# Kernel tuning notes

Measured on AMD Instinct MI355X. Metric: run time of the kernel, lower is better.

## Reference

```python
import jax, jax.numpy as jnp
import numpy as np

L = 4          # num_layers
D = 512        # d_model
NH = 8         # num_heads
DH = 64        # d_head
DFF = 2048     # d_ff
EPS = 1e-5     # nn.LayerNorm default eps


def _layer_norm(x, g, b):
    m = x.mean(axis=-1, keepdims=True)
    v = ((x - m) ** 2).mean(axis=-1, keepdims=True)
    return (x - m) / jnp.sqrt(v + EPS) * g + b


def setup_inputs() -> dict:
    key = jax.random.key(0)
    ks = jax.random.split(key, 14)
    s = 0.02
    z = jax.random.normal(ks[0], (4, 16, D, 8, 8), dtype=jnp.float32)
    Wq = s * jax.random.normal(ks[1], (L, D, NH * DH), dtype=jnp.float32)
    Wk = s * jax.random.normal(ks[2], (L, D, NH * DH), dtype=jnp.float32)
    Wv = s * jax.random.normal(ks[3], (L, D, NH * DH), dtype=jnp.float32)
    Wo = s * jax.random.normal(ks[4], (L, NH * DH, D), dtype=jnp.float32)
    W1 = s * jax.random.normal(ks[5], (L, D, DFF), dtype=jnp.float32)
    b1 = jnp.zeros((L, DFF), dtype=jnp.float32)
    W2 = s * jax.random.normal(ks[6], (L, DFF, D), dtype=jnp.float32)
    b2 = jnp.zeros((L, D), dtype=jnp.float32)
    ln1_g = jnp.ones((L, D), dtype=jnp.float32)
    ln1_b = jnp.zeros((L, D), dtype=jnp.float32)
    ln2_g = jnp.ones((L, D), dtype=jnp.float32)
    ln2_b = jnp.zeros((L, D), dtype=jnp.float32)
    return {"z": z, "Wq": Wq, "Wk": Wk, "Wv": Wv, "Wo": Wo,
            "W1": W1, "b1": b1, "W2": W2, "b2": b2,
            "ln1_g": ln1_g, "ln1_b": ln1_b, "ln2_g": ln2_g, "ln2_b": ln2_b}


def _forward(z, Wq, Wk, Wv, Wo, W1, b1, W2, b2, ln1_g, ln1_b, ln2_g, ln2_b):
    B, T, Dm, H, W = z.shape
    N = H * W
    Tp = T * N  # T' = t*h*w
    # sinusoidal positional embedding over T' positions
    pos = jnp.arange(Tp, dtype=z.dtype)
    inv_freq = 1.0 / (10000.0 ** (jnp.arange(0, Dm, 2, dtype=z.dtype) / Dm))
    si = pos[:, None] * inv_freq[None, :]                 # (T', D/2)
    pos_emb = jnp.concatenate([jnp.sin(si), jnp.cos(si)], axis=-1)[:, None, :]  # (T',1,D)
    # rearrange 'b t d h w -> (t h w) b d'
    x = jnp.transpose(z, (1, 3, 4, 0, 2)).reshape(Tp, B, Dm)
    x = x + pos_emb
    # block-causal mask at block size N (True = masked)
    blk = jnp.arange(Tp) // N
    mask = blk[None, :] > blk[:, None]                    # (T'_q, T'_k)
    scale = 1.0 / np.sqrt(DH)
    outs = []
    for l in range(L):
        # post-lnorm multi-head attention (LN applied before residual add)
        q = (x @ Wq[l]).reshape(Tp, B, NH, DH)
        k = (x @ Wk[l]).reshape(Tp, B, NH, DH)
        v = (x @ Wv[l]).reshape(Tp, B, NH, DH)
        s = jnp.einsum('ibnd,jbnd->ijbn', q, k) * scale
        s = jnp.where(mask[:, :, None, None], -jnp.inf, s)
        p = jax.nn.softmax(s, axis=1)
        av = jnp.einsum('ijbn,jbnd->ibnd', p, v).reshape(Tp, B, NH * DH)
        attn = _layer_norm(av @ Wo[l], ln1_g[l], ln1_b[l])
        x = attn + x
        ff = _layer_norm(jax.nn.relu(x @ W1[l] + b1[l]) @ W2[l] + b2[l], ln2_g[l], ln2_b[l])
        x = ff + x
        outs.append(x)
    out = jnp.stack(outs, axis=1)                         # (T', L, B, D)
    # rearrange '(t h w) l b d -> b t l d h w'
    out = out.reshape(T, H, W, L, B, Dm)
    return jnp.transpose(out, (4, 0, 3, 5, 1, 2))


def reference(z, Wq, Wk, Wv, Wo, W1, b1, W2, b2, ln1_g, ln1_b, ln2_g, ln2_b):
    return _forward(z, Wq, Wk, Wv, Wo, W1, b1, W2, b2, ln1_g, ln1_b, ln2_g, ln2_b)
```

## Files before the change

### kernel.cpp

```cpp
#include <hip/hip_runtime.h>
#include <hip/hip_bf16.h>
#include <math.h>


#define TP 1024
#define BB 4
#define DD 512
#define DHEAD 64
#define DFF 2048
#define MROWS (TP*BB)
#define EPS 1e-5f
#define CSC 0.18033688011112042f

typedef __attribute__((ext_vector_type(8))) short bf16x8;
typedef __attribute__((ext_vector_type(4))) float f32x4;

__device__ __forceinline__ float b2f(unsigned short u) {
    union { unsigned int i; float f; } z; z.i = ((unsigned int)u) << 16; return z.f;
}
__device__ __forceinline__ unsigned short f2bu(float f) {
    __hip_bfloat16 h = __float2bfloat16(f);
    return *reinterpret_cast<unsigned short*>(&h);
}

#define WAITV0() asm volatile("s_waitcnt vmcnt(0)" ::: "memory")
#define WAITV4() asm volatile("s_waitcnt vmcnt(4)" ::: "memory")
#define WAITV8() asm volatile("s_waitcnt vmcnt(8)" ::: "memory")
#define WAITL0() asm volatile("s_waitcnt lgkmcnt(0)" ::: "memory")
__device__ __forceinline__ void hard_barrier() {
    __builtin_amdgcn_sched_barrier(0);
    __builtin_amdgcn_s_barrier();
    __builtin_amdgcn_sched_barrier(0);
}
#define GLOAD(gp, lp) __builtin_amdgcn_global_load_lds( \
    (const __attribute__((address_space(1))) void*)(gp), \
    (__attribute__((address_space(3))) void*)(lp), 16, 0, 0)

__global__ __launch_bounds__(256) void embed_kernel(const float* __restrict__ z,
                                                    float* __restrict__ x,
                                                    __hip_bfloat16* __restrict__ x_bf) {
    int idx = blockIdx.x * 256 + threadIdx.x;
    int d  = idx & 511;
    int rb = idx >> 9;
    int b  = rb & 3;
    int i  = rb >> 2;
    int t = i >> 6, h = (i >> 3) & 7, w = i & 7;
    float zv = z[((((size_t)b * 16 + t) * 512 + d) * 8 + h) * 8 + w];
    int j = d & 255;
    float freq = expf(-(float)(2 * j) * (9.210340371976184f / 512.0f));
    float si = (float)i * freq;
    float pe = (d < 256) ? sinf(si) : cosf(si);
    float v = zv + pe;
    x[idx] = v;
    x_bf[idx] = __float2bfloat16(v);
}

__global__ __launch_bounds__(256) void wt_convert(
    const float* __restrict__ s0, const float* __restrict__ s1,
    const float* __restrict__ s2, const float* __restrict__ s3,
    const float* __restrict__ s4, const float* __restrict__ s5,
    __hip_bfloat16* __restrict__ d0, __hip_bfloat16* __restrict__ d1,
    __hip_bfloat16* __restrict__ d2, __hip_bfloat16* __restrict__ d3,
    __hip_bfloat16* __restrict__ d4, __hip_bfloat16* __restrict__ d5) {
    __shared__ float tile[32][33];
    int b = blockIdx.x;
    const float* src; __hip_bfloat16* dst; int R, C, local, cbs;
    if (b < 1024) {
        int m = b >> 8; local = b & 255; R = 512; C = 512; cbs = 4;
        src = (m == 0) ? s0 : (m == 1) ? s1 : (m == 2) ? s2 : s3;
        dst = (m == 0) ? d0 : (m == 1) ? d1 : (m == 2) ? d2 : d3;
    } else if (b < 2048) {
        local = b - 1024; R = 512; C = 2048; cbs = 6; src = s4; dst = d4;
    } else {
        local = b - 2048; R = 2048; C = 512; cbs = 4; src = s5; dst = d5;
    }
    int bx = local & ((1 << cbs) - 1), by = local >> cbs;
    int tx = threadIdx.x & 31, ty = threadIdx.x >> 5;
#pragma unroll
    for (int j = 0; j < 4; ++j)
        tile[ty + j * 8][tx] = src[(size_t)(by * 32 + ty + j * 8) * C + bx * 32 + tx];
    __syncthreads();
#pragma unroll
    for (int j = 0; j < 4; ++j)
        dst[(size_t)(bx * 32 + ty + j * 8) * R + by * 32 + tx] =
            __float2bfloat16(tile[tx][ty + j * 8]);
}

template<bool BIAS, bool RELU, bool OUT_BF16>
__global__ __launch_bounds__(256) void gemm_k(const __hip_bfloat16* __restrict__ A,
                                              const __hip_bfloat16* __restrict__ Bt,
                                              const float* __restrict__ bias,
                                              void* __restrict__ Cout,
                                              int N, int K, int ntx) {
    __shared__ __hip_bfloat16 As[2][128 * 32];
    __shared__ __hip_bfloat16 Bs[2][128 * 32];

    const int lb = blockIdx.x;
    const int wg = (lb & 7) * (gridDim.x >> 3) + (lb >> 3);
    const int m0 = (wg / ntx) * 128;
    const int n0 = (wg % ntx) * 128;

    const int tid  = threadIdx.x;
    const int wave = tid >> 6;
    const int lane = tid & 63;
    const int lr   = lane & 15;
    const int lk   = (lane >> 4) << 3;
    const int wr   = (wave >> 1) * 64;
    const int wc   = (wave & 1) * 64;

    f32x4 acc[4][4];
#pragma unroll
    for (int i = 0; i < 4; ++i)
#pragma unroll
        for (int j = 0; j < 4; ++j) acc[i][j] = (f32x4){0.f, 0.f, 0.f, 0.f};

    const int c0 = tid, c1 = tid + 256;
    const __hip_bfloat16* a0 = A  + (size_t)(m0 + (c0 >> 2)) * K + ((c0 & 3) << 3);
    const __hip_bfloat16* a1 = A  + (size_t)(m0 + (c1 >> 2)) * K + ((c1 & 3) << 3);
    const __hip_bfloat16* b0 = Bt + (size_t)(n0 + (c0 >> 2)) * K + ((c0 & 3) << 3);
    const __hip_bfloat16* b1 = Bt + (size_t)(n0 + (c1 >> 2)) * K + ((c1 & 3) << 3);
    const int o0 = wave * 512, o1 = 2048 + wave * 512;

    GLOAD(a0, &As[0][o0]); GLOAD(a1, &As[0][o1]);
    GLOAD(b0, &Bs[0][o0]); GLOAD(b1, &Bs[0][o1]);
    WAITV0();
    hard_barrier();

    for (int k0 = 0; k0 < K; k0 += 32) {
        const int buf = (k0 >> 5) & 1;
        if (k0 + 32 < K) {
            GLOAD(a0 + k0 + 32, &As[buf ^ 1][o0]); GLOAD(a1 + k0 + 32, &As[buf ^ 1][o1]);
            GLOAD(b0 + k0 + 32, &Bs[buf ^ 1][o0]); GLOAD(b1 + k0 + 32, &Bs[buf ^ 1][o1]);
        }
        bf16x8 af[4], bfv[4];
#pragma unroll
        for (int i = 0; i < 4; ++i)
            af[i] = *reinterpret_cast<const bf16x8*>(&As[buf][(size_t)(wr + i * 16 + lr) * 32 + lk]);
#pragma unroll
        for (int j = 0; j < 4; ++j)
            bfv[j] = *reinterpret_cast<const bf16x8*>(&Bs[buf][(size_t)(wc + j * 16 + lr) * 32 + lk]);
#pragma unroll
        for (int i = 0; i < 4; ++i)
#pragma unroll
            for (int j = 0; j < 4; ++j)
                acc[i][j] = __builtin_amdgcn_mfma_f32_16x16x32_bf16(af[i], bfv[j], acc[i][j], 0, 0, 0);
        WAITV0();
        hard_barrier();
    }

#pragma unroll
    for (int j = 0; j < 4; ++j) {
        int col = n0 + wc + j * 16 + lr;
        float bv = BIAS ? bias[col] : 0.0f;
#pragma unroll
        for (int i = 0; i < 4; ++i) {
            int row = m0 + wr + i * 16 + ((lane >> 4) << 2);
#pragma unroll
            for (int r = 0; r < 4; ++r) {
                float v = acc[i][j][r] + bv;
                if (RELU) v = fmaxf(v, 0.0f);
                if (OUT_BF16)
                    ((unsigned short*)Cout)[(size_t)(row + r) * N + col] = f2bu(v);
                else
                    ((float*)Cout)[(size_t)(row + r) * N + col] = v;
            }
        }
    }
}

template<bool BIAS, bool RELU, bool OUT_BF16>
__device__ __forceinline__ void gemm64_body(const __hip_bfloat16* __restrict__ A,
                                            const __hip_bfloat16* __restrict__ Bt,
                                            const float* __restrict__ bias,
                                            void* __restrict__ Cout, int K,
                                            float scale,
                                            __hip_bfloat16* As, __hip_bfloat16* Bs) {
    const int lb = blockIdx.x;
    const int wg = (lb & 7) * (gridDim.x >> 3) + (lb >> 3);
    const int m0 = (wg >> 3) * 64;
    const int n0 = (wg & 7) * 64;

    const int tid  = threadIdx.x;
    const int wave = tid >> 6;
    const int lane = tid & 63;
    const int lr   = lane & 15;
    const int hi   = lane >> 4;
    const int lk   = hi << 3;
    const int wr   = (wave >> 1) * 32;
    const int wc   = (wave & 1) * 32;

    f32x4 acc[2][2];
#pragma unroll
    for (int i = 0; i < 2; ++i)
#pragma unroll
        for (int j = 0; j < 2; ++j) acc[i][j] = (f32x4){0.f, 0.f, 0.f, 0.f};

    const __hip_bfloat16* ag = A  + (size_t)(m0 + (tid >> 2)) * K + ((tid & 3) << 3);
    const __hip_bfloat16* bg = Bt + (size_t)(n0 + (tid >> 2)) * K + ((tid & 3) << 3);
    const int wo = wave * 512;

    GLOAD(ag, As + wo); GLOAD(bg, Bs + wo);
    WAITV0();
    hard_barrier();

    for (int k0 = 0; k0 < K; k0 += 32) {
        const int buf = (k0 >> 5) & 1;
        if (k0 + 32 < K) {
            GLOAD(ag + k0 + 32, As + (buf ^ 1) * 2048 + wo);
            GLOAD(bg + k0 + 32, Bs + (buf ^ 1) * 2048 + wo);
        }
        const __hip_bfloat16* Ab = As + buf * 2048;
        const __hip_bfloat16* Bb = Bs + buf * 2048;
        bf16x8 af[2], bfv[2];
#pragma unroll
        for (int i = 0; i < 2; ++i)
            af[i] = *reinterpret_cast<const bf16x8*>(&Ab[(size_t)(wr + i * 16 + lr) * 32 + lk]);
#pragma unroll
        for (int j = 0; j < 2; ++j)
            bfv[j] = *reinterpret_cast<const bf16x8*>(&Bb[(size_t)(wc + j * 16 + lr) * 32 + lk]);
#pragma unroll
        for (int i = 0; i < 2; ++i)
#pragma unroll
            for (int j = 0; j < 2; ++j)
                acc[i][j] = __builtin_amdgcn_mfma_f32_16x16x32_bf16(af[i], bfv[j], acc[i][j], 0, 0, 0);
        WAITV0();
        hard_barrier();
    }

#pragma unroll
    for (int j = 0; j < 2; ++j) {
        int col = n0 + wc + j * 16 + lr;
        float bv = BIAS ? bias[col] : 0.0f;
#pragma unroll
        for (int i = 0; i < 2; ++i) {
            int row = m0 + wr + i * 16 + (hi << 2);
#pragma unroll
            for (int r = 0; r < 4; ++r) {
                float v = acc[i][j][r] * scale + bv;
                if (RELU) v = fmaxf(v, 0.0f);
                if (OUT_BF16)
                    ((unsigned short*)Cout)[(size_t)(row + r) * 512 + col] = f2bu(v);
                else
                    ((float*)Cout)[(size_t)(row + r) * 512 + col] = v;
            }
        }
    }
}

template<bool BIAS, bool RELU, bool OUT_BF16>
__global__ __launch_bounds__(256) void gemm64_k(const __hip_bfloat16* __restrict__ A,
                                                const __hip_bfloat16* __restrict__ Bt,
                                                const float* __restrict__ bias,
                                                void* __restrict__ Cout, int K) {
    __shared__ __hip_bfloat16 As[2 * 64 * 32];
    __shared__ __hip_bfloat16 Bs[2 * 64 * 32];
    gemm64_body<BIAS, RELU, OUT_BF16>(A, Bt, bias, Cout, K, 1.0f, As, Bs);
}

__global__ __launch_bounds__(256) void gemm_qkv64(const __hip_bfloat16* __restrict__ A,
                                                  const __hip_bfloat16* __restrict__ B0,
                                                  const __hip_bfloat16* __restrict__ B1,
                                                  const __hip_bfloat16* __restrict__ B2,
                                                  __hip_bfloat16* __restrict__ C0,
                                                  __hip_bfloat16* __restrict__ C1,
                                                  __hip_bfloat16* __restrict__ C2) {
    __shared__ __hip_bfloat16 As[2 * 64 * 32];
    __shared__ __hip_bfloat16 Bs[2 * 64 * 32];
    int sel = blockIdx.z;
    const __hip_bfloat16* Bt = (sel == 0) ? B0 : (sel == 1) ? B1 : B2;
    __hip_bfloat16* C = (sel == 0) ? C0 : (sel == 1) ? C1 : C2;
    float scale = (sel == 0) ? CSC : 1.0f;
    gemm64_body<false, false, true>(A, Bt, nullptr, (void*)C, 512, scale, As, Bs);
}

__global__ __launch_bounds__(256) void transpose_v(const unsigned short* __restrict__ v,
                                                   unsigned short* __restrict__ vt) {
    __shared__ unsigned short t[64][72];
    const int kb = blockIdx.x;
    const int bn = blockIdx.y;
    const int b = bn >> 3, n = bn & 7;
    const int tid = threadIdx.x;
#pragma unroll
    for (int it = 0; it < 2; ++it) {
        int c = tid + it * 256;
        int row = c >> 3, d0 = (c & 7) * 8;
        const unsigned short* src =
            v + ((size_t)((kb * 64 + row) * 4 + b)) * 512 + n * 64 + d0;
        bf16x8 xv = *reinterpret_cast<const bf16x8*>(src);
#pragma unroll
        for (int e = 0; e < 8; ++e) t[row][d0 + e] = (unsigned short)xv[e];
    }
    __syncthreads();
#pragma unroll
    for (int it = 0; it < 2; ++it) {
        int c = tid + it * 256;
        int d = c >> 3, k0 = (c & 7) * 8;
        bf16x8 o;
#pragma unroll
        for (int e = 0; e < 8; ++e) o[e] = (short)t[k0 + e][d];
        *reinterpret_cast<bf16x8*>(vt + ((size_t)(bn * 64 + d)) * 1024 + kb * 64 + k0) = o;
    }
}

__device__ __forceinline__ int aswz(int row, int col) {
    return (row * 64 + col) ^ ((row & 7) << 3);
}

__device__ __forceinline__ void stage_tile(const unsigned short* gbase, int stride,
                                           unsigned short* lds, int wave, int tid) {
#pragma unroll
    for (int it = 0; it < 2; ++it) {
        int c = tid + it * 256;
        int row = c >> 3;
        int i = (c & 7) ^ (row & 7);
        const unsigned short* g = gbase + (size_t)row * stride + i * 8;
        __builtin_amdgcn_global_load_lds(
            (const __attribute__((address_space(1))) void*)g,
            (__attribute__((address_space(3))) void*)(lds + it * 2048 + wave * 512),
            16, 0, 0);
    }
}

__global__ __launch_bounds__(256) void attn_mfma(const unsigned short* __restrict__ q,
                                                 const unsigned short* __restrict__ k,
                                                 const unsigned short* __restrict__ vt,
                                                 unsigned short* __restrict__ av) {
    __shared__ unsigned short Qs[64 * 64];
    __shared__ unsigned short Ks[4][64 * 64];
    __shared__ unsigned short Vts[4][64 * 64];
    __shared__ unsigned short Ps[64 * 64];

    const int tid = threadIdx.x;
    const int wave = tid >> 6, lane = tid & 63;
    const int lr = lane & 15, hi = lane >> 4;
    const int wr = wave * 16;

    const int p = blockIdx.x;
    const int xcd = p & 7, idx = p >> 3;
    const int bn = xcd * 4 + (idx & 3);
    const int qb = 15 - (idx >> 2);
    const int b = bn >> 3, n = bn & 7;

    const unsigned short* kcol  = k  + (size_t)b * 512 + n * 64;
    const unsigned short* vtrow = vt + (size_t)(bn * 64) * 1024;

    stage_tile(q + ((size_t)(qb * 64) * 4 + b) * 512 + n * 64, 2048, Qs, wave, tid);
    stage_tile(kcol, 2048, Ks[0], wave, tid);
    stage_tile(vtrow, 1024, Vts[0], wave, tid);
    if (qb >= 1) {
        stage_tile(kcol + (size_t)64 * 2048, 2048, Ks[1], wave, tid);
        stage_tile(vtrow + 64, 1024, Vts[1], wave, tid);
    }
    if (qb >= 2) {
        stage_tile(kcol + (size_t)128 * 2048, 2048, Ks[2], wave, tid);
        stage_tile(vtrow + 128, 1024, Vts[2], wave, tid);
    }

    f32x4 o_acc[4], l_acc;
#pragma unroll
    for (int db = 0; db < 4; ++db) o_acc[db] = (f32x4){0.f, 0.f, 0.f, 0.f};
    l_acc = (f32x4){0.f, 0.f, 0.f, 0.f};

    bf16x8 onesf;
#pragma unroll
    for (int e = 0; e < 8; ++e) onesf[e] = (short)0x3F80;

    bf16x8 qf[2];

    for (int kb = 0; kb <= qb; ++kb) {
        const int ahead = (qb - kb >= 2) ? 2 : (qb - kb);
        if (ahead == 2) WAITV8();
        else if (ahead == 1) WAITV4();
        else WAITV0();
        hard_barrier();
        if (kb + 3 <= qb) {
            stage_tile(kcol + (size_t)(kb + 3) * 64 * 2048, 2048,
                       Ks[(kb + 3) & 3], wave, tid);
            stage_tile(vtrow + (kb + 3) * 64, 1024, Vts[(kb + 3) & 3], wave, tid);
        }
        if (kb == 0) {
#pragma unroll
            for (int ks = 0; ks < 2; ++ks)
                qf[ks] = *reinterpret_cast<const bf16x8*>(
                    (const unsigned short*)Qs + aswz(wr + lr, ks * 32 + hi * 8));
        }
        const unsigned short* Kb = Ks[kb & 3];
        const unsigned short* Vb = Vts[kb & 3];

        f32x4 sf[4];
#pragma unroll
        for (int jb = 0; jb < 4; ++jb) sf[jb] = (f32x4){0.f, 0.f, 0.f, 0.f};
        __builtin_amdgcn_s_setprio(1);
#pragma unroll
        for (int ks = 0; ks < 2; ++ks) {
            bf16x8 a = qf[ks];
#pragma unroll
            for (int jb = 0; jb < 4; ++jb) {
                bf16x8 kf = *reinterpret_cast<const bf16x8*>(
                    Kb + aswz(jb * 16 + lr, ks * 32 + hi * 8));
                sf[jb] = __builtin_amdgcn_mfma_f32_16x16x32_bf16(a, kf, sf[jb], 0, 0, 0);
            }
        }
        __builtin_amdgcn_s_setprio(0);

#pragma unroll
        for (int jb = 0; jb < 4; ++jb)
#pragma unroll
            for (int r = 0; r < 4; ++r) {
                float pe = exp2f(fminf(sf[jb][r], 100.0f));
                Ps[aswz(wr + 4 * hi + r, jb * 16 + lr)] = f2bu(pe);
            }
        WAITL0();
        hard_barrier();

        __builtin_amdgcn_s_setprio(1);
#pragma unroll
        for (int ks = 0; ks < 2; ++ks) {
            bf16x8 pf = *reinterpret_cast<const bf16x8*>(
                (const unsigned short*)Ps + aswz(wr + lr, ks * 32 + hi * 8));
            l_acc = __builtin_amdgcn_mfma_f32_16x16x32_bf16(pf, onesf, l_acc, 0, 0, 0);
#pragma unroll
            for (int db = 0; db < 4; ++db) {
                bf16x8 vf = *reinterpret_cast<const bf16x8*>(
                    Vb + aswz(db * 16 + lr, ks * 32 + hi * 8));
                o_acc[db] = __builtin_amdgcn_mfma_f32_16x16x32_bf16(pf, vf, o_acc[db], 0, 0, 0);
            }
        }
        __builtin_amdgcn_s_setprio(0);
    }

#pragma unroll
    for (int r = 0; r < 4; ++r) {
        float inv = 1.0f / l_acc[r];
        int row = qb * 64 + wr + 4 * hi + r;
#pragma unroll
        for (int db = 0; db < 4; ++db)
            av[((size_t)row * 4 + b) * 512 + n * 64 + db * 16 + lr] =
                f2bu(o_acc[db][r] * inv);
    }
}

__global__ __launch_bounds__(64) void add_ln_kernel(const float* __restrict__ y,
                                                    const float* __restrict__ g,
                                                    const float* __restrict__ bta,
                                                    float* __restrict__ x,
                                                    __hip_bfloat16* __restrict__ x_bf) {
    const int row = blockIdx.x;
    const int tid = threadIdx.x;
    const float* yr = y + (size_t)row * DD;
    float4 v0 = *reinterpret_cast<const float4*>(&yr[tid * 4]);
    float4 v1 = *reinterpret_cast<const float4*>(&yr[256 + tid * 4]);
    float s = v0.x + v0.y + v0.z + v0.w + v1.x + v1.y + v1.z + v1.w;
    float ss = v0.x * v0.x + v0.y * v0.y + v0.z * v0.z + v0.w * v0.w +
               v1.x * v1.x + v1.y * v1.y + v1.z * v1.z + v1.w * v1.w;
#pragma unroll
    for (int off = 32; off; off >>= 1) {
        s  += __shfl_xor(s, off);
        ss += __shfl_xor(ss, off);
    }
    float mean = s * (1.0f / 512.0f);
    float var = ss * (1.0f / 512.0f) - mean * mean;
    float rstd = rsqrtf(var + EPS);

    float* xr = x + (size_t)row * DD;
    float vals[8] = {v0.x, v0.y, v0.z, v0.w, v1.x, v1.y, v1.z, v1.w};
#pragma unroll
    for (int e = 0; e < 8; ++e) {
        int d = (e < 4) ? (tid * 4 + e) : (256 + tid * 4 + (e - 4));
        float nrm = (vals[e] - mean) * rstd * g[d] + bta[d];
        float xo = xr[d] + nrm;
        xr[d] = xo;
        x_bf[(size_t)row * DD + d] = __float2bfloat16(xo);
    }
}

__global__ __launch_bounds__(256) void out_transpose(const float* __restrict__ x,
                                                     float* __restrict__ out, int l) {
    __shared__ float tile[64][65];
    const int blk = blockIdx.x;
    const int dc = blk & 7;
    const int b  = (blk >> 3) & 3;
    const int t  = blk >> 5;
    const int tid = threadIdx.x;
#pragma unroll
    for (int it = 0; it < 4; ++it) {
        int c = tid + it * 256;
        int hw = c >> 4, f4 = c & 15;
        const float* src = x + (size_t)((t * 64 + hw) * 4 + b) * 512 + dc * 64 + f4 * 4;
        float4 v = *reinterpret_cast<const float4*>(src);
        tile[hw][f4 * 4 + 0] = v.x; tile[hw][f4 * 4 + 1] = v.y;
        tile[hw][f4 * 4 + 2] = v.z; tile[hw][f4 * 4 + 3] = v.w;
    }
    __syncthreads();
    size_t ob = (((size_t)(b * 16 + t) * 4 + l) * 512 + dc * 64) * 64;
#pragma unroll
    for (int it = 0; it < 4; ++it) {
        int c = tid + it * 256;
        int d = c >> 4, f4 = c & 15;
        float4 v = make_float4(tile[f4 * 4 + 0][d], tile[f4 * 4 + 1][d],
                               tile[f4 * 4 + 2][d], tile[f4 * 4 + 3][d]);
        *reinterpret_cast<float4*>(out + ob + (size_t)d * 64 + f4 * 4) = v;
    }
}

extern "C" void kernel_launch(void* const* d_in, const int* in_sizes, int n_in,
                              void* d_out, int out_size, void* d_ws, size_t ws_size,
                              hipStream_t stream) {
    const float* z    = (const float*)d_in[0];
    const float* Wq   = (const float*)d_in[1];
    const float* Wk   = (const float*)d_in[2];
    const float* Wv   = (const float*)d_in[3];
    const float* Wo   = (const float*)d_in[4];
    const float* W1   = (const float*)d_in[5];
    const float* b1   = (const float*)d_in[6];
    const float* W2   = (const float*)d_in[7];
    const float* b2   = (const float*)d_in[8];
    const float* ln1g = (const float*)d_in[9];
    const float* ln1b = (const float*)d_in[10];
    const float* ln2g = (const float*)d_in[11];
    const float* ln2b = (const float*)d_in[12];
    float* out = (float*)d_out;

    const size_t MB = 1u << 20;
    char* base = (char*)d_ws;
    float*          x     = (float*)(base);
    __hip_bfloat16* x_bf  = (__hip_bfloat16*)(base + 8  * MB);
    __hip_bfloat16* q_bf  = (__hip_bfloat16*)(base + 12 * MB);
    __hip_bfloat16* k_bf  = (__hip_bfloat16*)(base + 16 * MB);
    __hip_bfloat16* v_bf  = (__hip_bfloat16*)(base + 20 * MB);
    __hip_bfloat16* av_bf = (__hip_bfloat16*)(base + 24 * MB);
    float*          tmp   = (float*)(base + 28 * MB);
    __hip_bfloat16* wqt   = (__hip_bfloat16*)(base + 36 * MB);
    __hip_bfloat16* wkt   = wqt + 512 * 512;
    __hip_bfloat16* wvt   = wkt + 512 * 512;
    __hip_bfloat16* wot   = wvt + 512 * 512;
    __hip_bfloat16* w1t   = wot + 512 * 512;
    __hip_bfloat16* w2t   = w1t + 512 * 2048;
    __hip_bfloat16* ff1_bf = q_bf;
    unsigned short* vt    = (unsigned short*)tmp;

    embed_kernel<<<(TP * BB * DD) / 256, 256, 0, stream>>>(z, x, x_bf);

    for (int l = 0; l < 4; ++l) {
        wt_convert<<<3072, 256, 0, stream>>>(
            Wq + (size_t)l * 512 * 512, Wk + (size_t)l * 512 * 512,
            Wv + (size_t)l * 512 * 512, Wo + (size_t)l * 512 * 512,
            W1 + (size_t)l * 512 * 2048, W2 + (size_t)l * 2048 * 512,
            wqt, wkt, wvt, wot, w1t, w2t);

        gemm_qkv64<<<dim3(512, 1, 3), 256, 0, stream>>>(x_bf, wqt, wkt, wvt,
                                                        q_bf, k_bf, v_bf);

        transpose_v<<<dim3(16, 32), 256, 0, stream>>>((const unsigned short*)v_bf, vt);

        attn_mfma<<<512, 256, 0, stream>>>(
            (const unsigned short*)q_bf, (const unsigned short*)k_bf,
            vt, (unsigned short*)av_bf);

        gemm64_k<false, false, false><<<512, 256, 0, stream>>>(
            av_bf, wot, nullptr, (void*)tmp, 512);
        add_ln_kernel<<<MROWS, 64, 0, stream>>>(tmp, ln1g + l * 512, ln1b + l * 512,
                                                x, x_bf);

        gemm_k<true, true, true><<<512, 256, 0, stream>>>(
            x_bf, w1t, b1 + l * 2048, (void*)ff1_bf, 2048, 512, 16);
        gemm64_k<true, false, false><<<512, 256, 0, stream>>>(
            ff1_bf, w2t, b2 + l * 512, (void*)tmp, 2048);
        add_ln_kernel<<<MROWS, 64, 0, stream>>>(tmp, ln2g + l * 512, ln2b + l * 512,
                                                x, x_bf);
        out_transpose<<<512, 256, 0, stream>>>(x, out, l);
    }
}
```

Before: 479.5 us.

## Fuse output GEMMs with LayerNorm, swizzle LDS, batch weight conversion, tile embed

Replaces the Wo and W2 GEMMs plus their separate add+LayerNorm kernels with a fused GEMM+LN kernel. Each block computes 16 full rows of 512 columns and normalizes them in registers, so the fp32 temporary round-trip and two launches per layer go away. It also XOR-swizzles the LDS layout in all GEMMs to cut bank conflicts, converts all four layers' weights in one launch before the loop, and rewrites the embedding as a shared-memory tiled transpose with vectorized stores. The fused kernel launches only 256 blocks, each loading the full 512-wide B tile per k-step, which may reduce parallelism and increase weight traffic.

```diff
diff --git a/kernel.cpp b/kernel.cpp
--- a/kernel.cpp
+++ b/kernel.cpp
@@ -36,43 +36,67 @@
     (const __attribute__((address_space(1))) void*)(gp), \
     (__attribute__((address_space(3))) void*)(lp), 16, 0, 0)
 
+__device__ __forceinline__ int fsw(int row) { return (row ^ (row >> 2)) & 3; }
+
 __global__ __launch_bounds__(256) void embed_kernel(const float* __restrict__ z,
                                                     float* __restrict__ x,
                                                     __hip_bfloat16* __restrict__ x_bf) {
-    int idx = blockIdx.x * 256 + threadIdx.x;
-    int d  = idx & 511;
-    int rb = idx >> 9;
-    int b  = rb & 3;
-    int i  = rb >> 2;
-    int t = i >> 6, h = (i >> 3) & 7, w = i & 7;
-    float zv = z[((((size_t)b * 16 + t) * 512 + d) * 8 + h) * 8 + w];
-    int j = d & 255;
-    float freq = expf(-(float)(2 * j) * (9.210340371976184f / 512.0f));
-    float si = (float)i * freq;
-    float pe = (d < 256) ? sinf(si) : cosf(si);
-    float v = zv + pe;
-    x[idx] = v;
-    x_bf[idx] = __float2bfloat16(v);
+    __shared__ float tile[64][65];
+    const int blk = blockIdx.x;
+    const int dc = blk & 7, b = (blk >> 3) & 3, t = blk >> 5;
+    const int tid = threadIdx.x;
+#pragma unroll
+    for (int it = 0; it < 4; ++it) {
+        int idx = it * 256 + tid;
+        int d_i = idx >> 4, hw4 = (idx & 15) * 4;
+        int d = dc * 64 + d_i;
+        float4 v = *reinterpret_cast<const float4*>(
+            z + ((size_t)((b * 16 + t) * 512 + d)) * 64 + hw4);
+        int j = d & 255;
+        float freq = expf(-(float)(2 * j) * (9.210340371976184f / 512.0f));
+        int i0 = t * 64 + hw4;
+#pragma unroll
+        for (int e = 0; e < 4; ++e) {
+            float si = (float)(i0 + e) * freq;
+            float pe = (d < 256) ? sinf(si) : cosf(si);
+            tile[d_i][hw4 + e] = ((&v.x)[e]) + pe;
+        }
+    }
+    __syncthreads();
+#pragma unroll
+    for (int it = 0; it < 4; ++it) {
+        int idx = it * 256 + tid;
+        int hw_o = idx >> 4, dq = (idx & 15) * 4;
+        int row = (t * 64 + hw_o) * 4 + b;
+        float4 v = make_float4(tile[dq][hw_o], tile[dq + 1][hw_o],
+                               tile[dq + 2][hw_o], tile[dq + 3][hw_o]);
+        *reinterpret_cast<float4*>(x + (size_t)row * 512 + dc * 64 + dq) = v;
+        ushort4 u;
+        u.x = f2bu(v.x); u.y = f2bu(v.y); u.z = f2bu(v.z); u.w = f2bu(v.w);
+        *reinterpret_cast<ushort4*>((unsigned short*)x_bf + (size_t)row * 512 + dc * 64 + dq) = u;
+    }
 }
 
 __global__ __launch_bounds__(256) void wt_convert(
-    const float* __restrict__ s0, const float* __restrict__ s1,
-    const float* __restrict__ s2, const float* __restrict__ s3,
-    const float* __restrict__ s4, const float* __restrict__ s5,
-    __hip_bfloat16* __restrict__ d0, __hip_bfloat16* __restrict__ d1,
-    __hip_bfloat16* __restrict__ d2, __hip_bfloat16* __restrict__ d3,
-    __hip_bfloat16* __restrict__ d4, __hip_bfloat16* __restrict__ d5) {
+    const float* __restrict__ Wq, const float* __restrict__ Wk,
+    const float* __restrict__ Wv, const float* __restrict__ Wo,
+    const float* __restrict__ W1, const float* __restrict__ W2,
+    __hip_bfloat16* __restrict__ wall) {
     __shared__ float tile[32][33];
+    const int l = blockIdx.y;
+    __hip_bfloat16* wl = wall + (size_t)l * (4 * 512 * 512 + 2 * 512 * 2048);
     int b = blockIdx.x;
     const float* src; __hip_bfloat16* dst; int R, C, local, cbs;
     if (b < 1024) {
         int m = b >> 8; local = b & 255; R = 512; C = 512; cbs = 4;
-        src = (m == 0) ? s0 : (m == 1) ? s1 : (m == 2) ? s2 : s3;
-        dst = (m == 0) ? d0 : (m == 1) ? d1 : (m == 2) ? d2 : d3;
+        src = ((m == 0) ? Wq : (m == 1) ? Wk : (m == 2) ? Wv : Wo) + (size_t)l * 512 * 512;
+        dst = wl + m * 512 * 512;
     } else if (b < 2048) {
-        local = b - 1024; R = 512; C = 2048; cbs = 6; src = s4; dst = d4;
+        local = b - 1024; R = 512; C = 2048; cbs = 6;
+        src = W1 + (size_t)l * 512 * 2048; dst = wl + 4 * 512 * 512;
     } else {
-        local = b - 2048; R = 2048; C = 512; cbs = 4; src = s5; dst = d5;
+        local = b - 2048; R = 2048; C = 512; cbs = 4;
+        src = W2 + (size_t)l * 2048 * 512; dst = wl + 4 * 512 * 512 + 512 * 2048;
     }
     int bx = local & ((1 << cbs) - 1), by = local >> cbs;
     int tx = threadIdx.x & 31, ty = threadIdx.x >> 5;
@@ -104,7 +128,8 @@
     const int wave = tid >> 6;
     const int lane = tid & 63;
     const int lr   = lane & 15;
-    const int lk   = (lane >> 4) << 3;
+    const int hi   = lane >> 4;
+    const int lk   = (hi ^ fsw(lr)) << 3;
     const int wr   = (wave >> 1) * 64;
     const int wc   = (wave & 1) * 64;
 
@@ -115,10 +140,10 @@
         for (int j = 0; j < 4; ++j) acc[i][j] = (f32x4){0.f, 0.f, 0.f, 0.f};
 
     const int c0 = tid, c1 = tid + 256;
-    const __hip_bfloat16* a0 = A  + (size_t)(m0 + (c0 >> 2)) * K + ((c0 & 3) << 3);
-    const __hip_bfloat16* a1 = A  + (size_t)(m0 + (c1 >> 2)) * K + ((c1 & 3) << 3);
-    const __hip_bfloat16* b0 = Bt + (size_t)(n0 + (c0 >> 2)) * K + ((c0 & 3) << 3);
-    const __hip_bfloat16* b1 = Bt + (size_t)(n0 + (c1 >> 2)) * K + ((c1 & 3) << 3);
+    const __hip_bfloat16* a0 = A  + (size_t)(m0 + (c0 >> 2)) * K + (((c0 & 3) ^ fsw(c0 >> 2)) << 3);
+    const __hip_bfloat16* a1 = A  + (size_t)(m0 + (c1 >> 2)) * K + (((c1 & 3) ^ fsw(c1 >> 2)) << 3);
+    const __hip_bfloat16* b0 = Bt + (size_t)(n0 + (c0 >> 2)) * K + (((c0 & 3) ^ fsw(c0 >> 2)) << 3);
+    const __hip_bfloat16* b1 = Bt + (size_t)(n0 + (c1 >> 2)) * K + (((c1 & 3) ^ fsw(c1 >> 2)) << 3);
     const int o0 = wave * 512, o1 = 2048 + wave * 512;
 
     GLOAD(a0, &As[0][o0]); GLOAD(a1, &As[0][o1]);
@@ -154,7 +179,7 @@
         float bv = BIAS ? bias[col] : 0.0f;
 #pragma unroll
         for (int i = 0; i < 4; ++i) {
-            int row = m0 + wr + i * 16 + ((lane >> 4) << 2);
+            int row = m0 + wr + i * 16 + (hi << 2);
 #pragma unroll
             for (int r = 0; r < 4; ++r) {
                 float v = acc[i][j][r] + bv;
@@ -168,10 +193,9 @@
     }
 }
 
-template<bool BIAS, bool RELU, bool OUT_BF16>
+template<bool OUT_BF16>
 __device__ __forceinline__ void gemm64_body(const __hip_bfloat16* __restrict__ A,
                                             const __hip_bfloat16* __restrict__ Bt,
-                                            const float* __restrict__ bias,
                                             void* __restrict__ Cout, int K,
                                             float scale,
                                             __hip_bfloat16* As, __hip_bfloat16* Bs) {
@@ -185,7 +209,7 @@
     const int lane = tid & 63;
     const int lr   = lane & 15;
     const int hi   = lane >> 4;
-    const int lk   = hi << 3;
+    const int lk   = (hi ^ fsw(lr)) << 3;
     const int wr   = (wave >> 1) * 32;
     const int wc   = (wave & 1) * 32;
 
@@ -195,8 +219,8 @@
 #pragma unroll
         for (int j = 0; j < 2; ++j) acc[i][j] = (f32x4){0.f, 0.f, 0.f, 0.f};
 
-    const __hip_bfloat16* ag = A  + (size_t)(m0 + (tid >> 2)) * K + ((tid & 3) << 3);
-    const __hip_bfloat16* bg = Bt + (size_t)(n0 + (tid >> 2)) * K + ((tid & 3) << 3);
+    const __hip_bfloat16* ag = A  + (size_t)(m0 + (tid >> 2)) * K + (((tid & 3) ^ fsw(tid >> 2)) << 3);
+    const __hip_bfloat16* bg = Bt + (size_t)(n0 + (tid >> 2)) * K + (((tid & 3) ^ fsw(tid >> 2)) << 3);
     const int wo = wave * 512;
 
     GLOAD(ag, As + wo); GLOAD(bg, Bs + wo);
@@ -230,14 +254,12 @@
 #pragma unroll
     for (int j = 0; j < 2; ++j) {
         int col = n0 + wc + j * 16 + lr;
-        float bv = BIAS ? bias[col] : 0.0f;
 #pragma unroll
         for (int i = 0; i < 2; ++i) {
             int row = m0 + wr + i * 16 + (hi << 2);
 #pragma unroll
             for (int r = 0; r < 4; ++r) {
-                float v = acc[i][j][r] * scale + bv;
-                if (RELU) v = fmaxf(v, 0.0f);
+                float v = acc[i][j][r] * scale;
                 if (OUT_BF16)
                     ((unsigned short*)Cout)[(size_t)(row + r) * 512 + col] = f2bu(v);
                 else
@@ -245,16 +267,6 @@
             }
         }
     }
-}
-
-template<bool BIAS, bool RELU, bool OUT_BF16>
-__global__ __launch_bounds__(256) void gemm64_k(const __hip_bfloat16* __restrict__ A,
-                                                const __hip_bfloat16* __restrict__ Bt,
-                                                const float* __restrict__ bias,
-                                                void* __restrict__ Cout, int K) {
-    __shared__ __hip_bfloat16 As[2 * 64 * 32];
-    __shared__ __hip_bfloat16 Bs[2 * 64 * 32];
-    gemm64_body<BIAS, RELU, OUT_BF16>(A, Bt, bias, Cout, K, 1.0f, As, Bs);
 }
 
 __global__ __launch_bounds__(256) void gemm_qkv64(const __hip_bfloat16* __restrict__ A,
@@ -270,7 +282,125 @@
     const __hip_bfloat16* Bt = (sel == 0) ? B0 : (sel == 1) ? B1 : B2;
     __hip_bfloat16* C = (sel == 0) ? C0 : (sel == 1) ? C1 : C2;
     float scale = (sel == 0) ? CSC : 1.0f;
-    gemm64_body<false, false, true>(A, Bt, nullptr, (void*)C, 512, scale, As, Bs);
+    gemm64_body<true>(A, Bt, (void*)C, 512, scale, As, Bs);
+}
+
+template<bool BIAS>
+__global__ __launch_bounds__(256) void gemm_ln_k(const __hip_bfloat16* __restrict__ A,
+                                                 const __hip_bfloat16* __restrict__ Bt,
+                                                 const float* __restrict__ bias,
+                                                 const float* __restrict__ g,
+                                                 const float* __restrict__ beta,
+                                                 float* __restrict__ x,
+                                                 __hip_bfloat16* __restrict__ x_bf,
+                                                 int K) {
+    __shared__ __hip_bfloat16 As[2][16 * 32];
+    __shared__ __hip_bfloat16 Bs[2][512 * 32];
+    __shared__ float red[2][4][16];
+
+    const int lb = blockIdx.x;
+    const int wg = (lb & 7) * 32 + (lb >> 3);
+    const int m0 = wg * 16;
+
+    const int tid  = threadIdx.x;
+    const int wave = tid >> 6;
+    const int lane = tid & 63;
+    const int lr   = lane & 15;
+    const int hi   = lane >> 4;
+    const int lk   = (hi ^ fsw(lr)) << 3;
+
+    f32x4 acc[8];
+#pragma unroll
+    for (int j = 0; j < 8; ++j) acc[j] = (f32x4){0.f, 0.f, 0.f, 0.f};
+
+    const __hip_bfloat16* bg[8];
+#pragma unroll
+    for (int it = 0; it < 8; ++it) {
+        int c = it * 256 + tid;
+        bg[it] = Bt + (size_t)(c >> 2) * K + (((c & 3) ^ fsw(c >> 2)) << 3);
+    }
+    const __hip_bfloat16* ag =
+        A + (size_t)(m0 + (lane >> 2)) * K + (((lane & 3) ^ fsw(lane >> 2)) << 3);
+
+#pragma unroll
+    for (int it = 0; it < 8; ++it)
+        GLOAD(bg[it], &Bs[0][(it * 256 + wave * 64) * 8]);
+    if (wave == 0) GLOAD(ag, &As[0][0]);
+    WAITV0();
+    hard_barrier();
+
+    for (int k0 = 0; k0 < K; k0 += 32) {
+        const int buf = (k0 >> 5) & 1;
+        if (k0 + 32 < K) {
+#pragma unroll
+            for (int it = 0; it < 8; ++it)
+                GLOAD(bg[it] + k0 + 32, &Bs[buf ^ 1][(it * 256 + wave * 64) * 8]);
+            if (wave == 0) GLOAD(ag + k0 + 32, &As[buf ^ 1][0]);
+        }
+        bf16x8 af = *reinterpret_cast<const bf16x8*>(&As[buf][(size_t)lr * 32 + lk]);
+        __builtin_amdgcn_s_setprio(1);
+#pragma unroll
+        for (int j = 0; j < 8; ++j) {
+            bf16x8 bf = *reinterpret_cast<const bf16x8*>(
+                &Bs[buf][(size_t)(wave * 128 + j * 16 + lr) * 32 + lk]);
+            acc[j] = __builtin_amdgcn_mfma_f32_16x16x32_bf16(af, bf, acc[j], 0, 0, 0);
+        }
+        __builtin_amdgcn_s_setprio(0);
+        WAITV0();
+        hard_barrier();
+    }
+
+    if (BIAS) {
+#pragma unroll
+        for (int j = 0; j < 8; ++j) {
+            float bv = bias[wave * 128 + j * 16 + lr];
+#pragma unroll
+            for (int r = 0; r < 4; ++r) acc[j][r] += bv;
+        }
+    }
+    float psum[4], psq[4];
+#pragma unroll
+    for (int r = 0; r < 4; ++r) {
+        float s = 0.f, ss = 0.f;
+#pragma unroll
+        for (int j = 0; j < 8; ++j) { s += acc[j][r]; ss += acc[j][r] * acc[j][r]; }
+#pragma unroll
+        for (int off = 1; off < 16; off <<= 1) {
+            s  += __shfl_xor(s, off);
+            ss += __shfl_xor(ss, off);
+        }
+        psum[r] = s; psq[r] = ss;
+    }
+    if (lr == 0) {
+#pragma unroll
+        for (int r = 0; r < 4; ++r) {
+            red[0][wave][hi * 4 + r] = psum[r];
+            red[1][wave][hi * 4 + r] = psq[r];
+        }
+    }
+    __syncthreads();
+    float mean[4], rstd[4];
+#pragma unroll
+    for (int r = 0; r < 4; ++r) {
+        int row = hi * 4 + r;
+        float s  = red[0][0][row] + red[0][1][row] + red[0][2][row] + red[0][3][row];
+        float ss = red[1][0][row] + red[1][1][row] + red[1][2][row] + red[1][3][row];
+        float m = s * (1.0f / 512.0f);
+        float v = ss * (1.0f / 512.0f) - m * m;
+        mean[r] = m; rstd[r] = rsqrtf(v + EPS);
+    }
+#pragma unroll
+    for (int j = 0; j < 8; ++j) {
+        int col = wave * 128 + j * 16 + lr;
+        float gv = g[col], bv = beta[col];
+#pragma unroll
+        for (int r = 0; r < 4; ++r) {
+            size_t off = (size_t)(m0 + hi * 4 + r) * 512 + col;
+            float xo = (acc[j][r] - mean[r]) * rstd[r] * gv + bv + x[off];
+            x[off] = xo;
+            ((unsigned short*)x_bf)[off] = f2bu(xo);
+        }
+    }
 }
 
 __global__ __launch_bounds__(256) void transpose_v(const unsigned short* __restrict__ v,
@@ -437,40 +567,6 @@
         for (int db = 0; db < 4; ++db)
             av[((size_t)row * 4 + b) * 512 + n * 64 + db * 16 + lr] =
                 f2bu(o_acc[db][r] * inv);
-    }
-}
-
-__global__ __launch_bounds__(64) void add_ln_kernel(const float* __restrict__ y,
-                                                    const float* __restrict__ g,
-                                                    const float* __restrict__ bta,
-                                                    float* __restrict__ x,
-                                                    __hip_bfloat16* __restrict__ x_bf) {
-    const int row = blockIdx.x;
-    const int tid = threadIdx.x;
-    const float* yr = y + (size_t)row * DD;
-    float4 v0 = *reinterpret_cast<const float4*>(&yr[tid * 4]);
-    float4 v1 = *reinterpret_cast<const float4*>(&yr[256 + tid * 4]);
-    float s = v0.x + v0.y + v0.z + v0.w + v1.x + v1.y + v1.z + v1.w;
-    float ss = v0.x * v0.x + v0.y * v0.y + v0.z * v0.z + v0.w * v0.w +
-               v1.x * v1.x + v1.y * v1.y + v1.z * v1.z + v1.w * v1.w;
-#pragma unroll
-    for (int off = 32; off; off >>= 1) {
-        s  += __shfl_xor(s, off);
-        ss += __shfl_xor(ss, off);
-    }
-    float mean = s * (1.0f / 512.0f);
-    float var = ss * (1.0f / 512.0f) - mean * mean;
-    float rstd = rsqrtf(var + EPS);
-
-    float* xr = x + (size_t)row * DD;
-    float vals[8] = {v0.x, v0.y, v0.z, v0.w, v1.x, v1.y, v1.z, v1.w};
-#pragma unroll
-    for (int e = 0; e < 8; ++e) {
-        int d = (e < 4) ? (tid * 4 + e) : (256 + tid * 4 + (e - 4));
-        float nrm = (vals[e] - mean) * rstd * g[d] + bta[d];
-        float xo = xr[d] + nrm;
-        xr[d] = xo;
-        x_bf[(size_t)row * DD + d] = __float2bfloat16(xo);
     }
 }
 
@@ -529,24 +625,23 @@
     __hip_bfloat16* k_bf  = (__hip_bfloat16*)(base + 16 * MB);
     __hip_bfloat16* v_bf  = (__hip_bfloat16*)(base + 20 * MB);
     __hip_bfloat16* av_bf = (__hip_bfloat16*)(base + 24 * MB);
-    float*          tmp   = (float*)(base + 28 * MB);
-    __hip_bfloat16* wqt   = (__hip_bfloat16*)(base + 36 * MB);
-    __hip_bfloat16* wkt   = wqt + 512 * 512;
-    __hip_bfloat16* wvt   = wkt + 512 * 512;
-    __hip_bfloat16* wot   = wvt + 512 * 512;
-    __hip_bfloat16* w1t   = wot + 512 * 512;
-    __hip_bfloat16* w2t   = w1t + 512 * 2048;
+    unsigned short* vt    = (unsigned short*)(base + 28 * MB);
+    __hip_bfloat16* wall  = (__hip_bfloat16*)(base + 36 * MB);
     __hip_bfloat16* ff1_bf = q_bf;
-    unsigned short* vt    = (unsigned short*)tmp;
-
-    embed_kernel<<<(TP * BB * DD) / 256, 256, 0, stream>>>(z, x, x_bf);
+
+    const size_t WL = 4 * 512 * 512 + 2 * 512 * 2048;
+
+    embed_kernel<<<512, 256, 0, stream>>>(z, x, x_bf);
+    wt_convert<<<dim3(3072, 4), 256, 0, stream>>>(Wq, Wk, Wv, Wo, W1, W2, wall);
 
     for (int l = 0; l < 4; ++l) {
-        wt_convert<<<3072, 256, 0, stream>>>(
-            Wq + (size_t)l * 512 * 512, Wk + (size_t)l * 512 * 512,
-            Wv + (size_t)l * 512 * 512, Wo + (size_t)l * 512 * 512,
-            W1 + (size_t)l * 512 * 2048, W2 + (size_t)l * 2048 * 512,
-            wqt, wkt, wvt, wot, w1t, w2t);
+        __hip_bfloat16* wl  = wall + (size_t)l * WL;
+        __hip_bfloat16* wqt = wl;
+        __hip_bfloat16* wkt = wqt + 512 * 512;
+        __hip_bfloat16* wvt = wkt + 512 * 512;
+        __hip_bfloat16* wot = wvt + 512 * 512;
+        __hip_bfloat16* w1t = wot + 512 * 512;
+        __hip_bfloat16* w2t = w1t + 512 * 2048;
 
         gemm_qkv64<<<dim3(512, 1, 3), 256, 0, stream>>>(x_bf, wqt, wkt, wvt,
                                                         q_bf, k_bf, v_bf);
@@ -557,17 +652,15 @@
             (const unsigned short*)q_bf, (const unsigned short*)k_bf,
             vt, (unsigned short*)av_bf);
 
-        gemm64_k<false, false, false><<<512, 256, 0, stream>>>(
-            av_bf, wot, nullptr, (void*)tmp, 512);
-        add_ln_kernel<<<MROWS, 64, 0, stream>>>(tmp, ln1g + l * 512, ln1b + l * 512,
-                                                x, x_bf);
+        gemm_ln_k<false><<<256, 256, 0, stream>>>(
+            av_bf, wot, nullptr, ln1g + l * 512, ln1b + l * 512, x, x_bf, 512);
 
         gemm_k<true, true, true><<<512, 256, 0, stream>>>(
             x_bf, w1t, b1 + l * 2048, (void*)ff1_bf, 2048, 512, 16);
-        gemm64_k<true, false, false><<<512, 256, 0, stream>>>(
-            ff1_bf, w2t, b2 + l * 512, (void*)tmp, 2048);
-        add_ln_kernel<<<MROWS, 64, 0, stream>>>(tmp, ln2g + l * 512, ln2b + l * 512,
-                                                x, x_bf);
+
+        gemm_ln_k<true><<<256, 256, 0, stream>>>(
+            ff1_bf, w2t, b2 + l * 512, ln2g + l * 512, ln2b + l * 512, x, x_bf, 2048);
+
         out_transpose<<<512, 256, 0, stream>>>(x, out, l);
     }
 }
```

New measurement: 650.9 us. +35.7%, slower.

## Swizzle GEMM LDS tiles, batch weight conversion, and coalesce embed transpose

Applied to the files above, without the earlier changes.

Applies an XOR swizzle to the k-chunk offset of the GEMM global-to-LDS loads and the matching fragment reads, to cut LDS bank conflicts. Converts the weights for all four layers in one launch into a per-layer workspace instead of one launch per layer. Rewrites the embedding kernel to use an LDS-tiled transpose with float4 loads and stores instead of strided scalar gathers. The cost is a larger weight workspace (about 24 MB) and extra index arithmetic in the GEMM loads.

```diff
diff --git a/kernel.cpp b/kernel.cpp
--- a/kernel.cpp
+++ b/kernel.cpp
@@ -36,43 +36,67 @@
     (const __attribute__((address_space(1))) void*)(gp), \
     (__attribute__((address_space(3))) void*)(lp), 16, 0, 0)
 
+__device__ __forceinline__ int fsw(int row) { return (row ^ (row >> 2)) & 3; }
+
 __global__ __launch_bounds__(256) void embed_kernel(const float* __restrict__ z,
                                                     float* __restrict__ x,
                                                     __hip_bfloat16* __restrict__ x_bf) {
-    int idx = blockIdx.x * 256 + threadIdx.x;
-    int d  = idx & 511;
-    int rb = idx >> 9;
-    int b  = rb & 3;
-    int i  = rb >> 2;
-    int t = i >> 6, h = (i >> 3) & 7, w = i & 7;
-    float zv = z[((((size_t)b * 16 + t) * 512 + d) * 8 + h) * 8 + w];
-    int j = d & 255;
-    float freq = expf(-(float)(2 * j) * (9.210340371976184f / 512.0f));
-    float si = (float)i * freq;
-    float pe = (d < 256) ? sinf(si) : cosf(si);
-    float v = zv + pe;
-    x[idx] = v;
-    x_bf[idx] = __float2bfloat16(v);
+    __shared__ float tile[64][65];
+    const int blk = blockIdx.x;
+    const int dc = blk & 7, b = (blk >> 3) & 3, t = blk >> 5;
+    const int tid = threadIdx.x;
+#pragma unroll
+    for (int it = 0; it < 4; ++it) {
+        int idx = it * 256 + tid;
+        int d_i = idx >> 4, hw4 = (idx & 15) * 4;
+        int d = dc * 64 + d_i;
+        float4 v = *reinterpret_cast<const float4*>(
+            z + ((size_t)((b * 16 + t) * 512 + d)) * 64 + hw4);
+        int j = d & 255;
+        float freq = expf(-(float)(2 * j) * (9.210340371976184f / 512.0f));
+        int i0 = t * 64 + hw4;
+#pragma unroll
+        for (int e = 0; e < 4; ++e) {
+            float si = (float)(i0 + e) * freq;
+            float pe = (d < 256) ? sinf(si) : cosf(si);
+            tile[d_i][hw4 + e] = ((&v.x)[e]) + pe;
+        }
+    }
+    __syncthreads();
+#pragma unroll
+    for (int it = 0; it < 4; ++it) {
+        int idx = it * 256 + tid;
+        int hw_o = idx >> 4, dq = (idx & 15) * 4;
+        int row = (t * 64 + hw_o) * 4 + b;
+        float4 v = make_float4(tile[dq][hw_o], tile[dq + 1][hw_o],
+                               tile[dq + 2][hw_o], tile[dq + 3][hw_o]);
+        *reinterpret_cast<float4*>(x + (size_t)row * 512 + dc * 64 + dq) = v;
+        ushort4 u;
+        u.x = f2bu(v.x); u.y = f2bu(v.y); u.z = f2bu(v.z); u.w = f2bu(v.w);
+        *reinterpret_cast<ushort4*>((unsigned short*)x_bf + (size_t)row * 512 + dc * 64 + dq) = u;
+    }
 }
 
 __global__ __launch_bounds__(256) void wt_convert(
-    const float* __restrict__ s0, const float* __restrict__ s1,
-    const float* __restrict__ s2, const float* __restrict__ s3,
-    const float* __restrict__ s4, const float* __restrict__ s5,
-    __hip_bfloat16* __restrict__ d0, __hip_bfloat16* __restrict__ d1,
-    __hip_bfloat16* __restrict__ d2, __hip_bfloat16* __restrict__ d3,
-    __hip_bfloat16* __restrict__ d4, __hip_bfloat16* __restrict__ d5) {
+    const float* __restrict__ Wq, const float* __restrict__ Wk,
+    const float* __restrict__ Wv, const float* __restrict__ Wo,
+    const float* __restrict__ W1, const float* __restrict__ W2,
+    __hip_bfloat16* __restrict__ wall) {
     __shared__ float tile[32][33];
+    const int l = blockIdx.y;
+    __hip_bfloat16* wl = wall + (size_t)l * (4 * 512 * 512 + 2 * 512 * 2048);
     int b = blockIdx.x;
     const float* src; __hip_bfloat16* dst; int R, C, local, cbs;
     if (b < 1024) {
         int m = b >> 8; local = b & 255; R = 512; C = 512; cbs = 4;
-        src = (m == 0) ? s0 : (m == 1) ? s1 : (m == 2) ? s2 : s3;
-        dst = (m == 0) ? d0 : (m == 1) ? d1 : (m == 2) ? d2 : d3;
+        src = ((m == 0) ? Wq : (m == 1) ? Wk : (m == 2) ? Wv : Wo) + (size_t)l * 512 * 512;
+        dst = wl + m * 512 * 512;
     } else if (b < 2048) {
-        local = b - 1024; R = 512; C = 2048; cbs = 6; src = s4; dst = d4;
+        local = b - 1024; R = 512; C = 2048; cbs = 6;
+        src = W1 + (size_t)l * 512 * 2048; dst = wl + 4 * 512 * 512;
     } else {
-        local = b - 2048; R = 2048; C = 512; cbs = 4; src = s5; dst = d5;
+        local = b - 2048; R = 2048; C = 512; cbs = 4;
+        src = W2 + (size_t)l * 2048 * 512; dst = wl + 4 * 512 * 512 + 512 * 2048;
     }
     int bx = local & ((1 << cbs) - 1), by = local >> cbs;
     int tx = threadIdx.x & 31, ty = threadIdx.x >> 5;
@@ -104,7 +128,8 @@
     const int wave = tid >> 6;
     const int lane = tid & 63;
     const int lr   = lane & 15;
-    const int lk   = (lane >> 4) << 3;
+    const int hi   = lane >> 4;
+    const int lk   = (hi ^ fsw(lr)) << 3;
     const int wr   = (wave >> 1) * 64;
     const int wc   = (wave & 1) * 64;
 
@@ -115,10 +140,10 @@
         for (int j = 0; j < 4; ++j) acc[i][j] = (f32x4){0.f, 0.f, 0.f, 0.f};
 
     const int c0 = tid, c1 = tid + 256;
-    const __hip_bfloat16* a0 = A  + (size_t)(m0 + (c0 >> 2)) * K + ((c0 & 3) << 3);
-    const __hip_bfloat16* a1 = A  + (size_t)(m0 + (c1 >> 2)) * K + ((c1 & 3) << 3);
-    const __hip_bfloat16* b0 = Bt + (size_t)(n0 + (c0 >> 2)) * K + ((c0 & 3) << 3);
-    const __hip_bfloat16* b1 = Bt + (size_t)(n0 + (c1 >> 2)) * K + ((c1 & 3) << 3);
+    const __hip_bfloat16* a0 = A  + (size_t)(m0 + (c0 >> 2)) * K + (((c0 & 3) ^ fsw(c0 >> 2)) << 3);
+    const __hip_bfloat16* a1 = A  + (size_t)(m0 + (c1 >> 2)) * K + (((c1 & 3) ^ fsw(c1 >> 2)) << 3);
+    const __hip_bfloat16* b0 = Bt + (size_t)(n0 + (c0 >> 2)) * K + (((c0 & 3) ^ fsw(c0 >> 2)) << 3);
+    const __hip_bfloat16* b1 = Bt + (size_t)(n0 + (c1 >> 2)) * K + (((c1 & 3) ^ fsw(c1 >> 2)) << 3);
     const int o0 = wave * 512, o1 = 2048 + wave * 512;
 
     GLOAD(a0, &As[0][o0]); GLOAD(a1, &As[0][o1]);
@@ -154,7 +179,7 @@
         float bv = BIAS ? bias[col] : 0.0f;
 #pragma unroll
         for (int i = 0; i < 4; ++i) {
-            int row = m0 + wr + i * 16 + ((lane >> 4) << 2);
+            int row = m0 + wr + i * 16 + (hi << 2);
 #pragma unroll
             for (int r = 0; r < 4; ++r) {
                 float v = acc[i][j][r] + bv;
@@ -185,7 +210,7 @@
     const int lane = tid & 63;
     const int lr   = lane & 15;
     const int hi   = lane >> 4;
-    const int lk   = hi << 3;
+    const int lk   = (hi ^ fsw(lr)) << 3;
     const int wr   = (wave >> 1) * 32;
     const int wc   = (wave & 1) * 32;
 
@@ -195,8 +220,8 @@
 #pragma unroll
         for (int j = 0; j < 2; ++j) acc[i][j] = (f32x4){0.f, 0.f, 0.f, 0.f};
 
-    const __hip_bfloat16* ag = A  + (size_t)(m0 + (tid >> 2)) * K + ((tid & 3) << 3);
-    const __hip_bfloat16* bg = Bt + (size_t)(n0 + (tid >> 2)) * K + ((tid & 3) << 3);
+    const __hip_bfloat16* ag = A  + (size_t)(m0 + (tid >> 2)) * K + (((tid & 3) ^ fsw(tid >> 2)) << 3);
+    const __hip_bfloat16* bg = Bt + (size_t)(n0 + (tid >> 2)) * K + (((tid & 3) ^ fsw(tid >> 2)) << 3);
     const int wo = wave * 512;
 
     GLOAD(ag, As + wo); GLOAD(bg, Bs + wo);
@@ -530,23 +555,23 @@
     __hip_bfloat16* v_bf  = (__hip_bfloat16*)(base + 20 * MB);
     __hip_bfloat16* av_bf = (__hip_bfloat16*)(base + 24 * MB);
     float*          tmp   = (float*)(base + 28 * MB);
-    __hip_bfloat16* wqt   = (__hip_bfloat16*)(base + 36 * MB);
-    __hip_bfloat16* wkt   = wqt + 512 * 512;
-    __hip_bfloat16* wvt   = wkt + 512 * 512;
-    __hip_bfloat16* wot   = wvt + 512 * 512;
-    __hip_bfloat16* w1t   = wot + 512 * 512;
-    __hip_bfloat16* w2t   = w1t + 512 * 2048;
+    __hip_bfloat16* wall  = (__hip_bfloat16*)(base + 36 * MB);
     __hip_bfloat16* ff1_bf = q_bf;
     unsigned short* vt    = (unsigned short*)tmp;
 
-    embed_kernel<<<(TP * BB * DD) / 256, 256, 0, stream>>>(z, x, x_bf);
+    const size_t WL = 4 * 512 * 512 + 2 * 512 * 2048;
+
+    embed_kernel<<<512, 256, 0, stream>>>(z, x, x_bf);
+    wt_convert<<<dim3(3072, 4), 256, 0, stream>>>(Wq, Wk, Wv, Wo, W1, W2, wall);
 
     for (int l = 0; l < 4; ++l) {
-        wt_convert<<<3072, 256, 0, stream>>>(
-            Wq + (size_t)l * 512 * 512, Wk + (size_t)l * 512 * 512,
-            Wv + (size_t)l * 512 * 512, Wo + (size_t)l * 512 * 512,
-            W1 + (size_t)l * 512 * 2048, W2 + (size_t)l * 2048 * 512,
-            wqt, wkt, wvt, wot, w1t, w2t);
+        __hip_bfloat16* wl  = wall + (size_t)l * WL;
+        __hip_bfloat16* wqt = wl;
+        __hip_bfloat16* wkt = wqt + 512 * 512;
+        __hip_bfloat16* wvt = wkt + 512 * 512;
+        __hip_bfloat16* wot = wvt + 512 * 512;
+        __hip_bfloat16* w1t = wot + 512 * 512;
+        __hip_bfloat16* w2t = w1t + 512 * 2048;
 
         gemm_qkv64<<<dim3(512, 1, 3), 256, 0, stream>>>(x_bf, wqt, wkt, wvt,
                                                         q_bf, k_bf, v_bf);
```

Result: faster. 465.2 us (-3.0%).
